# Performance work log

Hardware: AMD Instinct MI355X
Metric: run time of the kernel (lower is better)

The kernel has to match this reference:

```python
import math
import jax, jax.numpy as jnp
import numpy as np

V, D, H, VD, QD, T, HIS, CDD, B = 50000, 300, 16, 16, 200, 20, 50, 5, 256
REPR = H * VD
SCALE = 1.0 / math.sqrt(D)  # original always scales by sqrt(embedding_dim)


def _mhsa_pool(x, Wq, Wv, Wk, bk, qvec):
    """Multi-head self-attention + additive (query-vector) attention pooling.
    x: [B, N, S, F]; Wq: [H, F, F]; Wv: [H, F, VD]; Wk: [REPR, QD]; bk: [QD]; qvec: [QD].
    Returns pooled representation [B, N, REPR].
    Faithful to the per-head loop: heads batched via a leading H axis; concat order
    of per-head value outputs == flatten of (H, VD).
    """
    b, n, s, f = x.shape
    q = jnp.einsum('bnsf,hfe->bhnse', x, Wq)                 # per-head query projection
    attn = jax.nn.softmax(jnp.einsum('bhnse,bnte->bhnst', q, x) * SCALE, axis=-1)
    o = jnp.einsum('bhnst,bntf->bhnsf', attn, x)
    val = jnp.einsum('bhnsf,hfv->bnshv', o, Wv).reshape(b, n, s, H * VD)  # [B,N,S,REPR]
    key = jnp.tanh(val @ Wk + bk)                            # [B,N,S,QD]
    w = jax.nn.softmax(jnp.einsum('q,bnsq->bns', qvec, key) * SCALE, axis=-1)
    return jnp.einsum('bns,bnsr->bnr', w, val)               # [B,N,REPR]


def setup_inputs() -> dict:
    key = jax.random.key(0)
    ks = jax.random.split(key, 13)
    f32 = jnp.float32
    return {
        'candidate_title': jax.random.randint(ks[0], (B, CDD, T), 0, V),
        'clicked_title': jax.random.randint(ks[1], (B, HIS, T), 0, V),
        'embedding': jax.random.normal(ks[2], (V, D), f32) * 0.1,
        'Wq_w': jax.random.normal(ks[3], (H, D, D), f32) * (1.0 / math.sqrt(D)),
        'Wv_w': jax.random.normal(ks[4], (H, D, VD), f32) * (1.0 / math.sqrt(D)),
        'Wk_w': jax.random.normal(ks[5], (REPR, QD), f32) * (1.0 / math.sqrt(REPR)),
        'bk_w': jnp.zeros((QD,), f32),
        'query_words': jax.random.normal(ks[6], (QD,), f32),
        'Wq_n': jax.random.normal(ks[7], (H, REPR, REPR), f32) * (1.0 / math.sqrt(REPR)),
        'Wv_n': jax.random.normal(ks[8], (H, REPR, VD), f32) * (1.0 / math.sqrt(REPR)),
        'Wk_n': jax.random.normal(ks[9], (REPR, QD), f32) * (1.0 / math.sqrt(REPR)),
        'bk_n': jnp.zeros((QD,), f32),
        'query_news': jax.random.normal(ks[10], (QD,), f32),
    }


def reference(candidate_title, clicked_title, embedding, Wq_w, Wv_w, Wk_w, bk_w,
              query_words, Wq_n, Wv_n, Wk_n, bk_n, query_news):
    # news encoder (dropout is identity in eval)
    cdd_emb = embedding[candidate_title]                     # [B,CDD,T,D]
    cdd_reprs = _mhsa_pool(cdd_emb, Wq_w, Wv_w, Wk_w, bk_w, query_words)  # [B,CDD,REPR]
    his_emb = embedding[clicked_title]                       # [B,HIS,T,D]
    his_reprs = _mhsa_pool(his_emb, Wq_w, Wv_w, Wk_w, bk_w, query_words)  # [B,HIS,REPR]
    # user encoder: news-level MHSA + additive pooling over history
    user_repr = _mhsa_pool(his_reprs[:, None], Wq_n, Wv_n, Wk_n, bk_n, query_news)[:, 0]  # [B,REPR]
    # click predictor: dot product, log-softmax over candidates (cdd_size > 1)
    score = jnp.einsum('bcr,br->bc', cdd_reprs, user_repr)   # [B,CDD]
    return jax.nn.log_softmax(score, axis=1)
```

## Files before the change

### kernel.cpp

```cpp
#include <hip/hip_runtime.h>
#include <hip/hip_bf16.h>
#include <math.h>

#define NB 256
#define CDD 5
#define HIS 50
#define NITEMS 55
#define TT 20
#define DD 300
#define NH 16
#define VDIM 16
#define RP 256
#define QDIM 200
#define SCALEF 0.057735026918962584f

typedef __attribute__((ext_vector_type(8)))  short bf16x8;
typedef __attribute__((ext_vector_type(4)))  short short4v;
typedef __attribute__((ext_vector_type(4)))  float f32x4;
typedef __attribute__((ext_vector_type(16))) float f32x16;

#define MFMA16(a,b,c) __builtin_amdgcn_mfma_f32_16x16x32_bf16((a),(b),(c),0,0,0)
#define MFMA32(a,b,c) __builtin_amdgcn_mfma_f32_32x32x16_bf16((a),(b),(c),0,0,0)

__device__ __forceinline__ ushort f2bf(float f) {
    union { float f; unsigned u; } c; c.f = f;
    unsigned u = c.u;
    return (ushort)((u + 0x7fffu + ((u >> 16) & 1u)) >> 16);
}
__device__ __forceinline__ float bf2f(ushort h) {
    union { unsigned u; float f; } c; c.u = ((unsigned)h) << 16;
    return c.f;
}

#define XS  328
#define QS  136
#define VS  264
#define XVS 264
#define XV7 136

__global__ __launch_bounds__(256)
void prep_wqa(const float* __restrict__ Wq, ushort* __restrict__ WqA)
{
    const int TOT = 16 * 102400;
    for (int idx = blockIdx.x * 256 + threadIdx.x; idx < TOT; idx += gridDim.x * 256) {
        const int h  = idx / 102400;
        int r  = idx - h * 102400;
        const int et = r / 10240;  r -= et * 10240;
        const int ks = r / 512;    r -= ks * 512;
        const int ei = r >> 4, ki = r & 15;
        const int e = et * 32 + ei, f = ks * 16 + ki;
        const float v = (e < 300 && f < 300) ? Wq[(h * 300 + f) * 300 + e] : 0.f;
        WqA[idx] = f2bf(v);
    }
}

__global__ __launch_bounds__(256)
void transpose_pad(const float* __restrict__ src, ushort* __restrict__ dst,
                   int R, int C, int src_ld, int Rp, int Cv,
                   long src_ss, long dst_ss)
{
    __shared__ float T[32][33];
    const int r0 = blockIdx.x * 32;
    const int c0 = blockIdx.y * 32;
    const float* s = src + blockIdx.z * src_ss;
    ushort* d = dst + blockIdx.z * dst_ss;
    const int i = threadIdx.x >> 3;
    const int j4 = (threadIdx.x & 7) * 4;
#pragma unroll
    for (int t = 0; t < 4; ++t) {
        const int r = r0 + i, c = c0 + j4 + t;
        T[i][j4 + t] = (r < R && c < C) ? s[(long)r * src_ld + c] : 0.f;
    }
    __syncthreads();
#pragma unroll
    for (int t = 0; t < 4; ++t) {
        const int orow = c0 + i;
        const int ocol = r0 + j4 + t;
        if (orow < Cv && ocol < Rp)
            d[(long)orow * Rp + ocol] = f2bf(T[j4 + t][i]);
    }
}

__global__ __launch_bounds__(256)
void prep_ev(const float* __restrict__ E, const ushort* __restrict__ WvT,
             ushort* __restrict__ EV)
{
    __shared__ ushort Ebf[64 * XS];
    const int tid = threadIdx.x;
    const int r0 = blockIdx.x * 64;
    for (int i = tid; i < (64 * XS) / 2; i += 256) ((unsigned*)Ebf)[i] = 0u;
    __syncthreads();
    for (int idx = tid; idx < 64 * 75; idx += 256) {
        const int row = idx / 75, q = idx - row * 75;
        const int vr = r0 + row;
        if (vr < 50000) {
            const float4 v = ((const float4*)E)[(long)vr * 75 + q];
            short4v p;
            p.x = (short)f2bf(v.x); p.y = (short)f2bf(v.y);
            p.z = (short)f2bf(v.z); p.w = (short)f2bf(v.w);
            *(short4v*)(Ebf + row * XS + q * 4) = p;
        }
    }
    __syncthreads();
    const int w = tid >> 6, l15 = tid & 15, lhi = (tid >> 4) & 3;
    const f32x4 z4 = {0.f, 0.f, 0.f, 0.f};
    for (int n = 0; n < 16; ++n) {
        f32x4 acc = z4;
#pragma unroll
        for (int ks = 0; ks < 10; ++ks) {
            const int off = ks * 32 + lhi * 8;
            const bf16x8 A = *(const bf16x8*)(Ebf + (16 * w + l15) * XS + off);
            const bf16x8 B = *(const bf16x8*)(WvT + (16 * n + l15) * 320 + off);
            acc = MFMA16(A, B, acc);
        }
#pragma unroll
        for (int r = 0; r < 4; ++r) {
            const int row = r0 + 16 * w + lhi * 4 + r;
            if (row < 50000) EV[(long)row * 256 + 16 * n + l15] = f2bf(acc[r]);
        }
    }
}

__device__ __forceinline__ f32x16 zero16() {
    f32x16 z;
#pragma unroll
    for (int i = 0; i < 16; ++i) z[i] = 0.f;
    return z;
}

__device__ __forceinline__ void qc_et3(const ushort* __restrict__ WqAh,
                                       const ushort* Xl, ushort* Qcl,
                                       int et, int jcol, int l31, int hi)
{
    f32x16 acc0 = zero16(), acc1 = zero16(), acc2 = zero16();
    const ushort* abase = WqAh + (et * 20) * 512 + l31 * 16 + hi * 8;
    bf16x8 Abuf[5];
#pragma unroll
    for (int i = 0; i < 5; ++i) Abuf[i] = *(const bf16x8*)(abase + i * 512);
    __builtin_amdgcn_s_setprio(1);
#pragma unroll
    for (int ks = 0; ks < 20; ++ks) {
        const bf16x8 A = Abuf[ks % 5];
        const int xoff = ks * 16 + hi * 8;
        const bf16x8 B0 = *(const bf16x8*)(Xl + (0 * 32 + l31) * XS + xoff);
        acc0 = MFMA32(A, B0, acc0);
        const bf16x8 B1 = *(const bf16x8*)(Xl + (1 * 32 + l31) * XS + xoff);
        acc1 = MFMA32(A, B1, acc1);
        const bf16x8 B2 = *(const bf16x8*)(Xl + (2 * 32 + l31) * XS + xoff);
        acc2 = MFMA32(A, B2, acc2);
        if (ks + 5 < 20) Abuf[ks % 5] = *(const bf16x8*)(abase + (ks + 5) * 512);
    }
    __builtin_amdgcn_s_setprio(0);
#pragma unroll
    for (int m = 0; m < 3; ++m) {
        f32x16 a;
        switch (m) { case 0: a = acc0; break; case 1: a = acc1; break; default: a = acc2; break; }
        if (m == 2 && l31 >= 16) continue;
        ushort* qrow = Qcl + (32 * m + l31) * QS + jcol * 32;
#pragma unroll
        for (int g = 0; g < 4; ++g) {
            short4v p;
            p.x = (short)f2bf(a[4 * g + 0]);
            p.y = (short)f2bf(a[4 * g + 1]);
            p.z = (short)f2bf(a[4 * g + 2]);
            p.w = (short)f2bf(a[4 * g + 3]);
            *(short4v*)(qrow + 8 * g + 4 * hi) = p;
        }
    }
}

template<int NT>
__device__ __forceinline__ void s_chunk(const ushort* Xl, const ushort* Qcl,
                                        f32x16& sacc, int ebase, int i20,
                                        int l31, int hi)
{
    const ushort* xr = Xl + (i20 + l31) * XS + ebase + hi * 8;
    const ushort* qr = Qcl + (i20 + l31) * QS + hi * 8;
#pragma unroll
    for (int kst = 0; kst < 2 * NT; ++kst) {
        const bf16x8 A = *(const bf16x8*)(xr + kst * 16);
        const bf16x8 B = *(const bf16x8*)(qr + kst * 16);
        sacc = MFMA32(A, B, sacc);
    }
}

#define POOLE 39296

__global__ __launch_bounds__(256, 2)
void word_encoder_v7(const int* __restrict__ cddT, const int* __restrict__ hisT,
                     const float* __restrict__ E,
                     const ushort* __restrict__ WqA, const ushort* __restrict__ EV,
                     const ushort* __restrict__ WkT,
                     const float* __restrict__ bk, const float* __restrict__ qv,
                     float* __restrict__ cddR, float* __restrict__ hisR)
{
    __shared__ ushort pool[POOLE];
    __shared__ float  wrf[80];
    __shared__ int    toks[80];
    ushort* Xbf = pool;
    ushort* Qc  = pool + 26240;
    ushort* XVT = pool + 37120;

    const int tid = threadIdx.x;
    const int w   = tid >> 6;
    const int l31 = tid & 31;
    const int hi  = (tid >> 5) & 1;
    const int l15 = tid & 15;
    const int lhi = (tid >> 4) & 3;
    const f32x4 z4 = {0.f, 0.f, 0.f, 0.f};
    const int item = w;
    const int i20  = item * 20;

    for (int i = tid; i < 26240 / 2; i += 256) ((unsigned*)Xbf)[i] = 0u;
    for (int i = tid; i < 2176 / 2; i += 256) ((unsigned*)XVT)[i] = 0u;
    if (tid < 80) {
        wrf[tid] = 0.f;
        const int it_l = tid / 20, t = tid - it_l * 20;
        const int gi = blockIdx.x * 4 + it_l;
        const int b = gi / NITEMS, it = gi - b * NITEMS;
        toks[tid] = (it < CDD) ? cddT[(b * CDD + it) * TT + t]
                               : hisT[(b * HIS + (it - CDD)) * TT + t];
    }
    __syncthreads();

    for (int idx = tid; idx < 80 * 38; idx += 256) {
        const int r = idx / 38, g = idx - r * 38;
        const long base = (long)toks[r] * 300 + g * 8;
        short4v p0, p1;
        if (g < 37) {
            const float4 v0 = *(const float4*)(E + base);
            const float4 v1 = *(const float4*)(E + base + 4);
            p0.x = (short)f2bf(v0.x); p0.y = (short)f2bf(v0.y);
            p0.z = (short)f2bf(v0.z); p0.w = (short)f2bf(v0.w);
            p1.x = (short)f2bf(v1.x); p1.y = (short)f2bf(v1.y);
            p1.z = (short)f2bf(v1.z); p1.w = (short)f2bf(v1.w);
        } else {
            const float4 v0 = *(const float4*)(E + base);
            p0.x = (short)f2bf(v0.x); p0.y = (short)f2bf(v0.y);
            p0.z = (short)f2bf(v0.z); p0.w = (short)f2bf(v0.w);
            p1.x = 0; p1.y = 0; p1.z = 0; p1.w = 0;
        }
        *(short4v*)(Xbf + r * XS + g * 8) = p0;
        *(short4v*)(Xbf + r * XS + g * 8 + 4) = p1;
    }
    __syncthreads();

    unsigned va0=0,va1=0,va2=0,va3=0,va4=0,va5=0,va6=0,va7=0;
    unsigned va8=0,va9=0,va10=0,va11=0,va12=0,va13=0,va14=0,va15=0;
    unsigned vb0=0,vb1=0,vb2=0,vb3=0,vb4=0,vb5=0,vb6=0,vb7=0;
    unsigned vb8=0,vb9=0,vb10=0,vb11=0,vb12=0,vb13=0,vb14=0,vb15=0;
    unsigned vc0=0,vc1=0,vc2=0,vc3=0,vc4=0,vc5=0,vc6=0,vc7=0;
    unsigned vc8=0,vc9=0,vc10=0,vc11=0,vc12=0,vc13=0,vc14=0,vc15=0;
    unsigned vd0=0,vd1=0,vd2=0,vd3=0,vd4=0,vd5=0,vd6=0,vd7=0;
    unsigned vd8=0,vd9=0,vd10=0,vd11=0,vd12=0,vd13=0,vd14=0,vd15=0;

#pragma unroll 1
    for (int h = 0; h < 16; ++h) {
        const ushort* WqAh = WqA + h * 102400;
        f32x16 sacc = zero16();

        if (tid < 160) {
            const int tok = tid >> 1, half = tid & 1;
            const int it2 = tok / 20, lt = tok - it2 * 20;
            const ushort4* src = (const ushort4*)(EV + (long)toks[tok] * 256 + h * 16 + half * 8);
            const ushort4 a = src[0], b2 = src[1];
            ushort* dst0 = XVT + (half * 8) * XV7 + it2 * 32 + lt;
            dst0[0 * XV7] = a.x;  dst0[1 * XV7] = a.y;
            dst0[2 * XV7] = a.z;  dst0[3 * XV7] = a.w;
            dst0[4 * XV7] = b2.x; dst0[5 * XV7] = b2.y;
            dst0[6 * XV7] = b2.z; dst0[7 * XV7] = b2.w;
        }
        qc_et3(WqAh, Xbf, Qc, w, w, l31, hi);
        __syncthreads();
        s_chunk<4>(Xbf, Qc, sacc, 0, i20, l31, hi);
        __syncthreads();

        qc_et3(WqAh, Xbf, Qc, 4 + w, w, l31, hi);
        __syncthreads();
        s_chunk<4>(Xbf, Qc, sacc, 128, i20, l31, hi);
        __syncthreads();

        if (w < 2) qc_et3(WqAh, Xbf, Qc, 8 + w, w, l31, hi);
        __syncthreads();
        s_chunk<2>(Xbf, Qc, sacc, 256, i20, l31, hi);
        __syncthreads();

        float pv[16];
        float vmax = -1e30f;
#pragma unroll
        for (int r = 0; r < 16; ++r) {
            const int t = (r & 3) + 8 * (r >> 2) + 4 * hi;
            const float v = (t < 20) ? sacc[r] * SCALEF : -1e30f;
            pv[r] = v;
            vmax = fmaxf(vmax, v);
        }
        vmax = fmaxf(vmax, __shfl_xor(vmax, 32, 64));
        float psum = 0.f;
#pragma unroll
        for (int r = 0; r < 16; ++r) {
            const int t = (r & 3) + 8 * (r >> 2) + 4 * hi;
            const float e = (t < 20) ? __expf(pv[r] - vmax) : 0.f;
            pv[r] = e;
            psum += e;
        }
        psum += __shfl_xor(psum, 32, 64);
        const float inv = 1.f / psum;
        ushort* Pl = Qc;
        if (l31 < 20) {
            ushort* prow = Pl + (i20 + l31) * QS;
#pragma unroll
            for (int r = 0; r < 16; ++r) {
                const int t = (r & 3) + 8 * (r >> 2) + 4 * hi;
                if (t < 20) prow[t] = f2bf(pv[r] * inv);
            }
        }
        asm volatile("s_waitcnt lgkmcnt(0)" ::: "memory");
        __builtin_amdgcn_sched_barrier(0);

        unsigned plo0, phi0, plo1, phi1;
        {
            const bf16x8 A0 = *(const bf16x8*)(Pl + (i20 + l15) * QS + lhi * 8);
            const bf16x8 B0 = *(const bf16x8*)(XVT + l15 * XV7 + item * 32 + lhi * 8);
            const f32x4 d0 = MFMA16(A0, B0, z4);
            const bf16x8 A1 = *(const bf16x8*)(Pl + (i20 + 16 + l15) * QS + lhi * 8);
            const f32x4 d1 = MFMA16(A1, B0, z4);
            plo0 = ((unsigned)f2bf(d0[1]) << 16) | (unsigned)f2bf(d0[0]);
            phi0 = ((unsigned)f2bf(d0[3]) << 16) | (unsigned)f2bf(d0[2]);
            plo1 = ((unsigned)f2bf(d1[1]) << 16) | (unsigned)f2bf(d1[0]);
            phi1 = ((unsigned)f2bf(d1[3]) << 16) | (unsigned)f2bf(d1[2]);
        }
#define PV_CASE(H) case H: va##H = plo0; vb##H = phi0; vc##H = plo1; vd##H = phi1; break;
        switch (h) {
            PV_CASE(0) PV_CASE(1) PV_CASE(2) PV_CASE(3)
            PV_CASE(4) PV_CASE(5) PV_CASE(6) PV_CASE(7)
            PV_CASE(8) PV_CASE(9) PV_CASE(10) PV_CASE(11)
            PV_CASE(12) PV_CASE(13) PV_CASE(14) PV_CASE(15)
        }
#undef PV_CASE
        __syncthreads();
    }

    ushort* Vlbf = Xbf;
    __syncthreads();
#pragma unroll 1
    for (int h2 = 0; h2 < 16; ++h2) {
        unsigned a = 0, b2 = 0, c = 0, d = 0;
#define UNP_CASE(H) case H: a = va##H; b2 = vb##H; c = vc##H; d = vd##H; break;
        switch (h2) {
            UNP_CASE(0) UNP_CASE(1) UNP_CASE(2) UNP_CASE(3)
            UNP_CASE(4) UNP_CASE(5) UNP_CASE(6) UNP_CASE(7)
            UNP_CASE(8) UNP_CASE(9) UNP_CASE(10) UNP_CASE(11)
            UNP_CASE(12) UNP_CASE(13) UNP_CASE(14) UNP_CASE(15)
        }
#undef UNP_CASE
        ushort* base0 = Vlbf + (i20 + lhi * 4) * VS + h2 * 16 + l15;
        base0[0 * VS] = (ushort)(a & 0xffffu);
        base0[1 * VS] = (ushort)(a >> 16);
        base0[2 * VS] = (ushort)(b2 & 0xffffu);
        base0[3 * VS] = (ushort)(b2 >> 16);
        if (lhi == 0) {
            ushort* base1 = Vlbf + (i20 + 16) * VS + h2 * 16 + l15;
            base1[0 * VS] = (ushort)(c & 0xffffu);
            base1[1 * VS] = (ushort)(c >> 16);
            base1[2 * VS] = (ushort)(d & 0xffffu);
            base1[3 * VS] = (ushort)(d >> 16);
        }
    }
    __syncthreads();

    for (int tile = w; tile < 65; tile += 4) {
        const int m = tile / 13, n = tile - m * 13;
        const int q = 16 * n + l15;
        const float bkq = (q < QDIM) ? bk[q] : 0.f;
        const float qvq = (q < QDIM) ? qv[q] : 0.f;
        f32x4 acc = z4;
#pragma unroll
        for (int ks = 0; ks < 8; ++ks) {
            const int off = ks * 32 + lhi * 8;
            const bf16x8 A = *(const bf16x8*)(Vlbf + (16 * m + l15) * VS + off);
            const bf16x8 B = *(const bf16x8*)(WkT + (16 * n + l15) * 256 + off);
            acc = MFMA16(A, B, acc);
        }
#pragma unroll
        for (int r = 0; r < 4; ++r) {
            float c = qvq * tanhf(acc[r] + bkq);
            c += __shfl_xor(c, 1, 64);
            c += __shfl_xor(c, 2, 64);
            c += __shfl_xor(c, 4, 64);
            c += __shfl_xor(c, 8, 64);
            if (l15 == 0) atomicAdd(&wrf[16 * m + lhi * 4 + r], c);
        }
    }
    __syncthreads();

    if (tid < 4) {
        const int i = tid;
        float m = -1e30f;
        for (int s = 0; s < 20; ++s) m = fmaxf(m, wrf[20 * i + s] * SCALEF);
        float sum = 0.f;
        for (int s = 0; s < 20; ++s) {
            const float e = __expf(wrf[20 * i + s] * SCALEF - m);
            wrf[20 * i + s] = e; sum += e;
        }
        const float invs = 1.f / sum;
        for (int s = 0; s < 20; ++s) wrf[20 * i + s] *= invs;
    }
    __syncthreads();

    for (int idx = tid; idx < 4 * 256; idx += 256) {
        const int i = idx >> 8, r = idx & 255;
        float s = 0.f;
#pragma unroll
        for (int t = 0; t < 20; ++t)
            s += wrf[20 * i + t] * bf2f(Vlbf[(20 * i + t) * VS + r]);
        const int gi = blockIdx.x * 4 + i;
        const int b = gi / NITEMS, it = gi - b * NITEMS;
        float* op = (it < CDD) ? (cddR + (b * CDD + it) * RP)
                               : (hisR + (b * HIS + (it - CDD)) * RP);
        op[r] = s;
    }
}

__device__ __forceinline__ void qc_et(const ushort* __restrict__ WqAh,
                                      const ushort* Xl, ushort* Qcl,
                                      int et, int jcol, int l31, int hi)
{
    f32x16 acc0 = zero16(), acc1 = zero16(), acc2 = zero16(),
           acc3 = zero16(), acc4 = zero16();
    const ushort* abase = WqAh + (et * 20) * 512 + l31 * 16 + hi * 8;
    bf16x8 Abuf[5];
#pragma unroll
    for (int i = 0; i < 5; ++i) Abuf[i] = *(const bf16x8*)(abase + i * 512);
    __builtin_amdgcn_s_setprio(1);
#pragma unroll
    for (int ks = 0; ks < 20; ++ks) {
        const bf16x8 A = Abuf[ks % 5];
        const int xoff = ks * 16 + hi * 8;
        const bf16x8 B0 = *(const bf16x8*)(Xl + (0 * 32 + l31) * XS + xoff);
        acc0 = MFMA32(A, B0, acc0);
        const bf16x8 B1 = *(const bf16x8*)(Xl + (1 * 32 + l31) * XS + xoff);
        acc1 = MFMA32(A, B1, acc1);
        const bf16x8 B2 = *(const bf16x8*)(Xl + (2 * 32 + l31) * XS + xoff);
        acc2 = MFMA32(A, B2, acc2);
        const bf16x8 B3 = *(const bf16x8*)(Xl + (3 * 32 + l31) * XS + xoff);
        acc3 = MFMA32(A, B3, acc3);
        const bf16x8 B4 = *(const bf16x8*)(Xl + (4 * 32 + l31) * XS + xoff);
        acc4 = MFMA32(A, B4, acc4);
        if (ks + 5 < 20) Abuf[ks % 5] = *(const bf16x8*)(abase + (ks + 5) * 512);
    }
    __builtin_amdgcn_s_setprio(0);
#pragma unroll
    for (int m = 0; m < 5; ++m) {
        f32x16 a;
        switch (m) {
            case 0: a = acc0; break; case 1: a = acc1; break;
            case 2: a = acc2; break; case 3: a = acc3; break;
            default: a = acc4; break;
        }
        ushort* qrow = Qcl + (32 * m + l31) * QS + jcol * 32;
#pragma unroll
        for (int g = 0; g < 4; ++g) {
            short4v p;
            p.x = (short)f2bf(a[4 * g + 0]);
            p.y = (short)f2bf(a[4 * g + 1]);
            p.z = (short)f2bf(a[4 * g + 2]);
            p.w = (short)f2bf(a[4 * g + 3]);
            *(short4v*)(qrow + 8 * g + 4 * hi) = p;
        }
    }
}

__global__ __launch_bounds__(512, 2)
void word_encoder_mfma(const int* __restrict__ cddT, const int* __restrict__ hisT,
                       const float* __restrict__ E,
                       const ushort* __restrict__ WqA, const ushort* __restrict__ WvT,
                       const ushort* __restrict__ WkT,
                       const float* __restrict__ bk, const float* __restrict__ qv,
                       float* __restrict__ cddR, float* __restrict__ hisR)
{
    __shared__ ushort Xbf[160 * XS];
    __shared__ ushort Qc[160 * QS];
    __shared__ ushort XVT[16 * XVS];
    __shared__ ushort toks[160];
    __shared__ float  wrf[160];

    const int tid = threadIdx.x;
    const int w   = tid >> 6;
    const int l31 = tid & 31;
    const int hi  = (tid >> 5) & 1;
    const int l15 = tid & 15;
    const int lhi = (tid >> 4) & 3;
    const f32x4 z4 = {0.f, 0.f, 0.f, 0.f};

    for (int i = tid; i < (160 * XS) / 2; i += 512) ((unsigned*)Xbf)[i] = 0u;
    for (int i = tid; i < (16 * XVS) / 2; i += 512) ((unsigned*)XVT)[i] = 0u;
    if (tid < 160) {
        wrf[tid] = 0.f;
        const int it_l = tid / 20, t = tid - it_l * 20;
        const int gi = blockIdx.x * 8 + it_l;
        const int b = gi / NITEMS, it = gi - b * NITEMS;
        const int tk = (it < CDD) ? cddT[(b * CDD + it) * TT + t]
                                  : hisT[(b * HIS + (it - CDD)) * TT + t];
        toks[tid] = (ushort)tk;
    }
    __syncthreads();

    for (int idx = tid; idx < 160 * 38; idx += 512) {
        const int r = idx / 38, g = idx - r * 38;
        const long base = (long)toks[r] * 300 + g * 8;
        short4v p0, p1;
        if (g < 37) {
            const float4 v0 = *(const float4*)(E + base);
            const float4 v1 = *(const float4*)(E + base + 4);
            p0.x = (short)f2bf(v0.x); p0.y = (short)f2bf(v0.y);
            p0.z = (short)f2bf(v0.z); p0.w = (short)f2bf(v0.w);
            p1.x = (short)f2bf(v1.x); p1.y = (short)f2bf(v1.y);
            p1.z = (short)f2bf(v1.z); p1.w = (short)f2bf(v1.w);
        } else {
            const float4 v0 = *(const float4*)(E + base);
            p0.x = (short)f2bf(v0.x); p0.y = (short)f2bf(v0.y);
            p0.z = (short)f2bf(v0.z); p0.w = (short)f2bf(v0.w);
            p1.x = 0; p1.y = 0; p1.z = 0; p1.w = 0;
        }
        *(short4v*)(Xbf + r * XS + g * 8) = p0;
        *(short4v*)(Xbf + r * XS + g * 8 + 4) = p1;
    }
    __syncthreads();

    unsigned va0=0,va1=0,va2=0,va3=0,va4=0,va5=0,va6=0,va7=0;
    unsigned va8=0,va9=0,va10=0,va11=0,va12=0,va13=0,va14=0,va15=0;
    unsigned vb0=0,vb1=0,vb2=0,vb3=0,vb4=0,vb5=0,vb6=0,vb7=0;
    unsigned vb8=0,vb9=0,vb10=0,vb11=0,vb12=0,vb13=0,vb14=0,vb15=0;
    unsigned vc0=0,vc1=0,vc2=0,vc3=0,vc4=0,vc5=0,vc6=0,vc7=0;
    unsigned vc8=0,vc9=0,vc10=0,vc11=0,vc12=0,vc13=0,vc14=0,vc15=0;
    unsigned vd0=0,vd1=0,vd2=0,vd3=0,vd4=0,vd5=0,vd6=0,vd7=0;
    unsigned vd8=0,vd9=0,vd10=0,vd11=0,vd12=0,vd13=0,vd14=0,vd15=0;

    const int item = w;
    const int i20  = item * 20;

#pragma unroll 1
    for (int h = 0; h < 16; ++h) {
        const ushort* WqAh = WqA + h * 102400;
        f32x16 sacc = zero16();

        if (w < 4) {
            qc_et(WqAh, Xbf, Qc, w, w, l31, hi);
        } else {
            for (int tt = w - 4; tt < 10; tt += 4) {
                f32x4 acc = z4;
#pragma unroll
                for (int ks = 0; ks < 10; ++ks) {
                    const int off = ks * 32 + lhi * 8;
                    const bf16x8 A = *(const bf16x8*)(WvT + (h * 16 + l15) * 320 + off);
                    const bf16x8 B = *(const bf16x8*)(Xbf + (tt * 16 + l15) * XS + off);
                    acc = MFMA16(A, B, acc);
                }
                const int t = tt * 16 + l15;
                const int it2 = t / 20, lt = t - it2 * 20;
#pragma unroll
                for (int r = 0; r < 4; ++r)
                    XVT[(lhi * 4 + r) * XVS + it2 * 32 + lt] = f2bf(acc[r]);
            }
        }
        __syncthreads();
        s_chunk<4>(Xbf, Qc, sacc, 0, i20, l31, hi);
        __syncthreads();

        if (w < 4) qc_et(WqAh, Xbf, Qc, 4 + w, w, l31, hi);
        __syncthreads();
        s_chunk<4>(Xbf, Qc, sacc, 128, i20, l31, hi);
        __syncthreads();

        if (w == 0 || w == 2) qc_et(WqAh, Xbf, Qc, 8 + (w >> 1), (w >> 1), l31, hi);
        __syncthreads();
        s_chunk<2>(Xbf, Qc, sacc, 256, i20, l31, hi);
        __syncthreads();

        float sv[16];
        float vmax = -1e30f;
#pragma unroll
        for (int r = 0; r < 16; ++r) {
            const int t = (r & 3) + 8 * (r >> 2) + 4 * hi;
            const float v = (t < 20) ? sacc[r] * SCALEF : -1e30f;
            sv[r] = v;
            vmax = fmaxf(vmax, v);
        }
        vmax = fmaxf(vmax, __shfl_xor(vmax, 32, 64));
        float psum = 0.f;
        float pv[16];
#pragma unroll
        for (int r = 0; r < 16; ++r) {
            const int t = (r & 3) + 8 * (r >> 2) + 4 * hi;
            const float e = (t < 20) ? __expf(sv[r] - vmax) : 0.f;
            pv[r] = e;
            psum += e;
        }
        psum += __shfl_xor(psum, 32, 64);
        const float inv = 1.f / psum;
        ushort* Pl = Qc;
        if (l31 < 20) {
            ushort* prow = Pl + (i20 + l31) * QS;
#pragma unroll
            for (int r = 0; r < 16; ++r) {
                const int t = (r & 3) + 8 * (r >> 2) + 4 * hi;
                if (t < 20) prow[t] = f2bf(pv[r] * inv);
            }
        }
        asm volatile("s_waitcnt lgkmcnt(0)" ::: "memory");
        __builtin_amdgcn_sched_barrier(0);

        unsigned plo0, phi0, plo1, phi1;
        {
            const bf16x8 A0 = *(const bf16x8*)(Pl + (i20 + l15) * QS + lhi * 8);
            const bf16x8 B0 = *(const bf16x8*)(XVT + l15 * XVS + item * 32 + lhi * 8);
            const f32x4 d0 = MFMA16(A0, B0, z4);
            const bf16x8 A1 = *(const bf16x8*)(Pl + (i20 + 16 + l15) * QS + lhi * 8);
            const f32x4 d1 = MFMA16(A1, B0, z4);
            plo0 = ((unsigned)f2bf(d0[1]) << 16) | (unsigned)f2bf(d0[0]);
            phi0 = ((unsigned)f2bf(d0[3]) << 16) | (unsigned)f2bf(d0[2]);
            plo1 = ((unsigned)f2bf(d1[1]) << 16) | (unsigned)f2bf(d1[0]);
            phi1 = ((unsigned)f2bf(d1[3]) << 16) | (unsigned)f2bf(d1[2]);
        }
#define PV_CASE(H) case H: va##H = plo0; vb##H = phi0; vc##H = plo1; vd##H = phi1; break;
        switch (h) {
            PV_CASE(0) PV_CASE(1) PV_CASE(2) PV_CASE(3)
            PV_CASE(4) PV_CASE(5) PV_CASE(6) PV_CASE(7)
            PV_CASE(8) PV_CASE(9) PV_CASE(10) PV_CASE(11)
            PV_CASE(12) PV_CASE(13) PV_CASE(14) PV_CASE(15)
        }
#undef PV_CASE
        __syncthreads();
    }

    ushort* Vlbf = Xbf;
    __syncthreads();
#pragma unroll 1
    for (int h2 = 0; h2 < 16; ++h2) {
        unsigned a = 0, b2 = 0, c = 0, d = 0;
#define UNP_CASE(H) case H: a = va##H; b2 = vb##H; c = vc##H; d = vd##H; break;
        switch (h2) {
            UNP_CASE(0) UNP_CASE(1) UNP_CASE(2) UNP_CASE(3)
            UNP_CASE(4) UNP_CASE(5) UNP_CASE(6) UNP_CASE(7)
            UNP_CASE(8) UNP_CASE(9) UNP_CASE(10) UNP_CASE(11)
            UNP_CASE(12) UNP_CASE(13) UNP_CASE(14) UNP_CASE(15)
        }
#undef UNP_CASE
        ushort* base0 = Vlbf + (i20 + lhi * 4) * VS + h2 * 16 + l15;
        base0[0 * VS] = (ushort)(a & 0xffffu);
        base0[1 * VS] = (ushort)(a >> 16);
        base0[2 * VS] = (ushort)(b2 & 0xffffu);
        base0[3 * VS] = (ushort)(b2 >> 16);
        if (lhi == 0) {
            ushort* base1 = Vlbf + (i20 + 16) * VS + h2 * 16 + l15;
            base1[0 * VS] = (ushort)(c & 0xffffu);
            base1[1 * VS] = (ushort)(c >> 16);
            base1[2 * VS] = (ushort)(d & 0xffffu);
            base1[3 * VS] = (ushort)(d >> 16);
        }
    }
    __syncthreads();

    for (int tile = w; tile < 130; tile += 8) {
        const int m = tile / 13, n = tile - m * 13;
        const int q = 16 * n + l15;
        const float bkq = (q < QDIM) ? bk[q] : 0.f;
        const float qvq = (q < QDIM) ? qv[q] : 0.f;
        f32x4 acc = z4;
#pragma unroll
        for (int ks = 0; ks < 8; ++ks) {
            const int off = ks * 32 + lhi * 8;
            const bf16x8 A = *(const bf16x8*)(Vlbf + (16 * m + l15) * VS + off);
            const bf16x8 B = *(const bf16x8*)(WkT + (16 * n + l15) * 256 + off);
            acc = MFMA16(A, B, acc);
        }
#pragma unroll
        for (int r = 0; r < 4; ++r) {
            float c = qvq * tanhf(acc[r] + bkq);
            c += __shfl_xor(c, 1, 64);
            c += __shfl_xor(c, 2, 64);
            c += __shfl_xor(c, 4, 64);
            c += __shfl_xor(c, 8, 64);
            if (l15 == 0) atomicAdd(&wrf[16 * m + lhi * 4 + r], c);
        }
    }
    __syncthreads();

    if (tid < 8) {
        const int i = tid;
        float m = -1e30f;
        for (int s = 0; s < 20; ++s) m = fmaxf(m, wrf[20 * i + s] * SCALEF);
        float sum = 0.f;
        for (int s = 0; s < 20; ++s) {
            const float e = __expf(wrf[20 * i + s] * SCALEF - m);
            wrf[20 * i + s] = e; sum += e;
        }
        const float invs = 1.f / sum;
        for (int s = 0; s < 20; ++s) wrf[20 * i + s] *= invs;
    }
    __syncthreads();

    for (int idx = tid; idx < 8 * 256; idx += 512) {
        const int i = idx >> 8, r = idx & 255;
        float s = 0.f;
#pragma unroll
        for (int t = 0; t < 20; ++t)
            s += wrf[20 * i + t] * bf2f(Vlbf[(20 * i + t) * VS + r]);
        const int gi = blockIdx.x * 8 + i;
        const int b = gi / NITEMS, it = gi - b * NITEMS;
        float* op = (it < CDD) ? (cddR + (b * CDD + it) * RP)
                               : (hisR + (b * HIS + (it - CDD)) * RP);
        op[r] = s;
    }
}

#define US   264
#define UTS  72
#define UXVS 72
#define UVS  264

__global__ __launch_bounds__(512, 2)
void user_encoder_mfma(const float* __restrict__ hisR,
                       const ushort* __restrict__ WqnT, const ushort* __restrict__ WvnT,
                       const ushort* __restrict__ WknT,
                       const float* __restrict__ bk, const float* __restrict__ qv,
                       float* __restrict__ userR)
{
    __shared__ ushort Xu[64 * US];
    __shared__ ushort Qu[64 * US];
    __shared__ ushort XVTu[16 * UXVS];
    __shared__ ushort Atu[64 * UTS];
    __shared__ ushort Vlu[64 * UVS];
    __shared__ float  wru[64];

    const int tid = threadIdx.x;
    const int w   = tid >> 6;
    const int l15 = tid & 15;
    const int lhi = (tid >> 4) & 3;
    const f32x4 z4 = {0.f, 0.f, 0.f, 0.f};

    for (int i = tid; i < (64 * US) / 2; i += 512) ((unsigned*)Xu)[i] = 0u;
    for (int i = tid; i < (64 * UTS) / 2; i += 512) ((unsigned*)Atu)[i] = 0u;
    for (int i = tid; i < (64 * UVS) / 2; i += 512) ((unsigned*)Vlu)[i] = 0u;
    if (tid < 64) wru[tid] = 0.f;
    __syncthreads();

    const float* xp = hisR + (long)blockIdx.x * (HIS * RP);
    for (int idx = tid; idx < 50 * 64; idx += 512) {
        const int s = idx >> 6, q = idx & 63;
        const float4 v = ((const float4*)xp)[idx];
        short4v p;
        p.x = (short)f2bf(v.x); p.y = (short)f2bf(v.y);
        p.z = (short)f2bf(v.z); p.w = (short)f2bf(v.w);
        *(short4v*)(Xu + s * US + q * 4) = p;
    }
    __syncthreads();

#pragma unroll 1
    for (int h = 0; h < 16; ++h) {
        const ushort* Wqh = WqnT + h * 65536;
        for (int t8 = w; t8 < 64; t8 += 8) {
            const int et = t8 >> 2, st = t8 & 3;
            f32x4 acc = z4;
#pragma unroll
            for (int ks = 0; ks < 8; ++ks) {
                const int off = ks * 32 + lhi * 8;
                const bf16x8 A = *(const bf16x8*)(Wqh + (16 * et + l15) * 256 + off);
                const bf16x8 B = *(const bf16x8*)(Xu + (16 * st + l15) * US + off);
                acc = MFMA16(A, B, acc);
            }
            short4v p;
            p.x = (short)f2bf(acc[0]); p.y = (short)f2bf(acc[1]);
            p.z = (short)f2bf(acc[2]); p.w = (short)f2bf(acc[3]);
            *(short4v*)(Qu + (16 * st + l15) * US + 16 * et + lhi * 4) = p;
        }
        __syncthreads();

        if (w < 4) {
            f32x4 a[4] = {z4, z4, z4, z4};
#pragma unroll
            for (int ks = 0; ks < 8; ++ks) {
                const int off = ks * 32 + lhi * 8;
                const bf16x8 qa = *(const bf16x8*)(Qu + (16 * w + l15) * US + off);
#pragma unroll
                for (int n = 0; n < 4; ++n)
                    a[n] = MFMA16(qa, *(const bf16x8*)(Xu + (16 * n + l15) * US + off), a[n]);
            }
#pragma unroll
            for (int r = 0; r < 4; ++r) {
                const int srow = 16 * w + lhi * 4 + r;
                float v[4];
                float m = -1e30f;
#pragma unroll
                for (int n = 0; n < 4; ++n) {
                    const int t = 16 * n + l15;
                    v[n] = (t < HIS) ? a[n][r] * SCALEF : -1e30f;
                    m = fmaxf(m, v[n]);
                }
                m = fmaxf(m, __shfl_xor(m, 1, 64));
                m = fmaxf(m, __shfl_xor(m, 2, 64));
                m = fmaxf(m, __shfl_xor(m, 4, 64));
                m = fmaxf(m, __shfl_xor(m, 8, 64));
                float p[4]; float sum = 0.f;
#pragma unroll
                for (int n = 0; n < 4; ++n) {
                    const int t = 16 * n + l15;
                    p[n] = (t < HIS) ? __expf(v[n] - m) : 0.f;
                    sum += p[n];
                }
                sum += __shfl_xor(sum, 1, 64);
                sum += __shfl_xor(sum, 2, 64);
                sum += __shfl_xor(sum, 4, 64);
                sum += __shfl_xor(sum, 8, 64);
                const float inv = 1.f / sum;
                if (srow < HIS) {
#pragma unroll
                    for (int n = 0; n < 4; ++n)
                        Atu[srow * UTS + 16 * n + l15] = f2bf(p[n] * inv);
                }
            }
        } else {
            const int j = w - 4;
            f32x4 acc = z4;
#pragma unroll
            for (int ks = 0; ks < 8; ++ks) {
                const int off = ks * 32 + lhi * 8;
                const bf16x8 A = *(const bf16x8*)(Xu + (16 * j + l15) * US + off);
                const bf16x8 B = *(const bf16x8*)(WvnT + (h * 16 + l15) * 256 + off);
                acc = MFMA16(A, B, acc);
            }
#pragma unroll
            for (int r = 0; r < 4; ++r)
                XVTu[l15 * UXVS + 16 * j + lhi * 4 + r] = f2bf(acc[r]);
        }
        __syncthreads();

        if (w < 4) {
            f32x4 acc = z4;
#pragma unroll
            for (int ks = 0; ks < 2; ++ks) {
                const int off = ks * 32 + lhi * 8;
                const bf16x8 A = *(const bf16x8*)(Atu + (16 * w + l15) * UTS + off);
                const bf16x8 B = *(const bf16x8*)(XVTu + l15 * UXVS + off);
                acc = MFMA16(A, B, acc);
            }
#pragma unroll
            for (int r = 0; r < 4; ++r) {
                const int srow = 16 * w + lhi * 4 + r;
                if (srow < HIS) Vlu[srow * UVS + h * 16 + l15] = f2bf(acc[r]);
            }
        }
        __syncthreads();
    }

    for (int tile = w; tile < 52; tile += 8) {
        const int m = tile / 13, n = tile - m * 13;
        const int q = 16 * n + l15;
        const float bkq = (q < QDIM) ? bk[q] : 0.f;
        const float qvq = (q < QDIM) ? qv[q] : 0.f;
        f32x4 acc = z4;
#pragma unroll
        for (int ks = 0; ks < 8; ++ks) {
            const int off = ks * 32 + lhi * 8;
            const bf16x8 A = *(const bf16x8*)(Vlu + (16 * m + l15) * UVS + off);
            const bf16x8 B = *(const bf16x8*)(WknT + (16 * n + l15) * 256 + off);
            acc = MFMA16(A, B, acc);
        }
#pragma unroll
        for (int r = 0; r < 4; ++r) {
            float c = qvq * tanhf(acc[r] + bkq);
            c += __shfl_xor(c, 1, 64);
            c += __shfl_xor(c, 2, 64);
            c += __shfl_xor(c, 4, 64);
            c += __shfl_xor(c, 8, 64);
            const int srow = 16 * m + lhi * 4 + r;
            if (l15 == 0 && srow < HIS) atomicAdd(&wru[srow], c);
        }
    }
    __syncthreads();
    if (tid == 0) {
        float m = -1e30f;
        for (int s = 0; s < HIS; ++s) m = fmaxf(m, wru[s] * SCALEF);
        float sum = 0.f;
        for (int s = 0; s < HIS; ++s) {
            const float e = __expf(wru[s] * SCALEF - m);
            wru[s] = e; sum += e;
        }
        const float inv = 1.f / sum;
        for (int s = 0; s < HIS; ++s) wru[s] *= inv;
    }
    __syncthreads();
    if (tid < 256) {
        float s = 0.f;
        for (int t = 0; t < HIS; ++t) s += wru[t] * bf2f(Vlu[t * UVS + tid]);
        userR[blockIdx.x * RP + tid] = s;
    }
}

#define FP2 257
#define CHW 129
__global__ __launch_bounds__(512)
void user_encoder_fp32(const float* __restrict__ hisR,
                       const float* __restrict__ Wq, const float* __restrict__ Wv,
                       const float* __restrict__ Wk, const float* __restrict__ bk,
                       const float* __restrict__ qv,
                       float* __restrict__ userR)
{
    __shared__ float Xs[HIS + 1][FP2];
    __shared__ float Vl[HIS][FP2];
    __shared__ float Qcf[HIS + 1][CHW];
    __shared__ float Sm[HIS][HIS + 2];
    __shared__ float XVh[HIS][VDIM + 1];
    __shared__ float wr[HIS];

    const int tid = threadIdx.x;
    const int b = blockIdx.x;
    const float* xp = hisR + b * (HIS * RP);
    for (int i = tid; i < HIS * RP; i += 512) {
        const int s = i >> 8, f = i & 255;
        Xs[s][f] = xp[i];
    }
    __syncthreads();
    for (int h = 0; h < NH; ++h) {
        for (int chunk = 0; chunk < 2; ++chunk) {
            __syncthreads();
            const int e0 = chunk * 128;
            {
                const int sg = tid >> 7, et = tid & 127;
                const int s0 = sg * 13 - (sg == 3 ? 1 : 0);
                const float* wq = Wq + h * (RP * RP) + e0 + et;
                float acc[13] = {};
                for (int f = 0; f < RP; ++f) {
                    const float w = wq[f * RP];
#pragma unroll
                    for (int i = 0; i < 13; ++i) acc[i] += Xs[s0 + i][f] * w;
                }
#pragma unroll
                for (int i = 0; i < 13; ++i) Qcf[s0 + i][et] = acc[i];
            }
            __syncthreads();
            for (int o = tid; o < HIS * HIS; o += 512) {
                const int s = o / HIS, t = o - s * HIS;
                float acc = (chunk == 0) ? 0.f : Sm[s][t];
                for (int e = 0; e < 128; ++e) acc += Qcf[s][e] * Xs[t][e0 + e];
                Sm[s][t] = acc;
            }
        }
        __syncthreads();
        if (tid < HIS) {
            const int s = tid;
            float m = -1e30f;
            for (int t = 0; t < HIS; ++t) m = fmaxf(m, Sm[s][t]);
            m *= SCALEF;
            float sum = 0.f;
            for (int t = 0; t < HIS; ++t) { const float e = __expf(Sm[s][t] * SCALEF - m); Sm[s][t] = e; sum += e; }
            const float inv = 1.f / sum;
            for (int t = 0; t < HIS; ++t) Sm[s][t] *= inv;
        }
        for (int o = tid; o < HIS * VDIM; o += 512) {
            const int t = o >> 4, v = o & 15;
            const float* wp = Wv + h * (RP * VDIM) + v;
            float acc = 0.f;
            for (int f = 0; f < RP; ++f) acc += Xs[t][f] * wp[f * VDIM];
            XVh[t][v] = acc;
        }
        __syncthreads();
        for (int o = tid; o < HIS * VDIM; o += 512) {
            const int s = o >> 4, v = o & 15;
            float acc = 0.f;
            for (int t = 0; t < HIS; ++t) acc += Sm[s][t] * XVh[t][v];
            Vl[s][h * VDIM + v] = acc;
        }
    }
    __syncthreads();
    {
        const int s = tid >> 3, g = tid & 7;
        float part = 0.f;
        if (s < HIS) {
            for (int q = g; q < QDIM; q += 8) {
                float acc = bk[q];
                const float* wp = Wk + q;
                for (int r = 0; r < RP; ++r) acc += Vl[s][r] * wp[r * QDIM];
                part += qv[q] * tanhf(acc);
            }
        }
        part += __shfl_down(part, 1, 64);
        part += __shfl_down(part, 2, 64);
        part += __shfl_down(part, 4, 64);
        if (g == 0 && s < HIS) wr[s] = part * SCALEF;
    }
    __syncthreads();
    if (tid == 0) {
        float m = -1e30f;
        for (int s = 0; s < HIS; ++s) m = fmaxf(m, wr[s]);
        float sum = 0.f;
        for (int s = 0; s < HIS; ++s) { const float e = __expf(wr[s] - m); wr[s] = e; sum += e; }
        const float inv = 1.f / sum;
        for (int s = 0; s < HIS; ++s) wr[s] *= inv;
    }
    __syncthreads();
    float* up = userR + b * RP;
    for (int r = tid; r < RP; r += 512) {
        float acc = 0.f;
        for (int s = 0; s < HIS; ++s) acc += wr[s] * Vl[s][r];
        up[r] = acc;
    }
}

__global__ __launch_bounds__(64)
void score_kernel(const float* __restrict__ cddR, const float* __restrict__ userR,
                  float* __restrict__ out)
{
    const int b = blockIdx.x;
    const int lane = threadIdx.x;
    const float* u = userR + b * RP;
    float sc[CDD];
#pragma unroll
    for (int c = 0; c < CDD; ++c) {
        const float* cr = cddR + (b * CDD + c) * RP;
        float part = 0.f;
        for (int r = lane; r < RP; r += 64) part += cr[r] * u[r];
#pragma unroll
        for (int off = 32; off > 0; off >>= 1) part += __shfl_down(part, off, 64);
        sc[c] = part;
    }
    if (lane == 0) {
        float m = -1e30f;
#pragma unroll
        for (int c = 0; c < CDD; ++c) m = fmaxf(m, sc[c]);
        float sum = 0.f;
#pragma unroll
        for (int c = 0; c < CDD; ++c) sum += __expf(sc[c] - m);
        const float lse = m + logf(sum);
#pragma unroll
        for (int c = 0; c < CDD; ++c) out[b * CDD + c] = sc[c] - lse;
    }
}

extern "C" void kernel_launch(void* const* d_in, const int* in_sizes, int n_in,
                              void* d_out, int out_size, void* d_ws, size_t ws_size,
                              hipStream_t stream) {
    const int*   cddT = (const int*)d_in[0];
    const int*   hisT = (const int*)d_in[1];
    const float* E    = (const float*)d_in[2];
    const float* Wq_w = (const float*)d_in[3];
    const float* Wv_w = (const float*)d_in[4];
    const float* Wk_w = (const float*)d_in[5];
    const float* bk_w = (const float*)d_in[6];
    const float* q_w  = (const float*)d_in[7];
    const float* Wq_n = (const float*)d_in[8];
    const float* Wv_n = (const float*)d_in[9];
    const float* Wk_n = (const float*)d_in[10];
    const float* bk_n = (const float*)d_in[11];
    const float* q_n  = (const float*)d_in[12];
    float* out = (float*)d_out;

    char* wsb = (char*)d_ws;
    float*  cdd_reprs = (float*)(wsb + 0);
    float*  his_reprs = (float*)(wsb + 1310720);
    float*  user_repr = (float*)(wsb + 14417920);
    ushort* WqA  = (ushort*)(wsb + 14680064);
    ushort* WvT  = (ushort*)(wsb + 17956864);
    ushort* WkT  = (ushort*)(wsb + 18120704);
    ushort* WqnT = (ushort*)(wsb + 18227200);
    ushort* WvnT = (ushort*)(wsb + 20324352);
    ushort* WknT = (ushort*)(wsb + 20455424);
    ushort* EV   = (ushort*)(wsb + 20561920);
    const bool mid  = ws_size >= 20561920ULL + 2335232ULL;
    const bool big  = ws_size >= 46161920ULL;

    prep_wqa<<<dim3(2048), 256, 0, stream>>>(Wq_w, WqA);
    transpose_pad<<<dim3(10, 1, 16), 256, 0, stream>>>(Wv_w, WvT, 300, 16, 16, 320, 16, 4800, 5120);
    transpose_pad<<<dim3(8, 7, 1), 256, 0, stream>>>(Wk_w, WkT, 256, 200, 200, 256, 208, 0, 0);
    if (mid) {
        transpose_pad<<<dim3(8, 8, 16), 256, 0, stream>>>(Wq_n, WqnT, 256, 256, 256, 256, 256, 65536, 65536);
        transpose_pad<<<dim3(8, 1, 16), 256, 0, stream>>>(Wv_n, WvnT, 256, 16, 16, 256, 16, 4096, 4096);
        transpose_pad<<<dim3(8, 7, 1), 256, 0, stream>>>(Wk_n, WknT, 256, 200, 200, 256, 208, 0, 0);
    }

    if (big) {
        prep_ev<<<dim3(782), 256, 0, stream>>>(E, WvT, EV);
        word_encoder_v7<<<dim3(NB * NITEMS / 4), dim3(256), 0, stream>>>(
            cddT, hisT, E, WqA, EV, WkT, bk_w, q_w, cdd_reprs, his_reprs);
    } else {
        word_encoder_mfma<<<dim3(NB * NITEMS / 8), dim3(512), 0, stream>>>(
            cddT, hisT, E, WqA, WvT, WkT, bk_w, q_w, cdd_reprs, his_reprs);
    }
    if (mid)
        user_encoder_mfma<<<dim3(NB), dim3(512), 0, stream>>>(
            his_reprs, WqnT, WvnT, WknT, bk_n, q_n, user_repr);
    else
        user_encoder_fp32<<<dim3(NB), dim3(512), 0, stream>>>(
            his_reprs, Wq_n, Wv_n, Wk_n, bk_n, q_n, user_repr);
    score_kernel<<<dim3(NB), dim3(64), 0, stream>>>(cdd_reprs, user_repr, out);
}
```

Measured before the change: 2.131 ms.

## Shrink word-encoder blocks to two items with 128 threads

Replaces the four-item, 256-thread word encoder with a two-item, 128-thread variant. Shared memory drops to about half, so more blocks can be resident per CU, and the Q projection now uses two MFMA tiles per wave, with the second tile padded from 8 rows. Row indices are remapped so padded lanes read duplicate rows, which removes wasted MFMA rows. The risk is that each block reloads the per-head Wq weights for fewer items, which lowers weight reuse and doubles the block count.

```diff
diff --git a/kernel.cpp b/kernel.cpp
--- a/kernel.cpp
+++ b/kernel.cpp
@@ -36,7 +36,7 @@
 #define QS  136
 #define VS  264
 #define XVS 264
-#define XV7 136
+#define XV8 72
 
 __global__ __launch_bounds__(256)
 void prep_wqa(const float* __restrict__ Wq, ushort* __restrict__ WqA)
@@ -128,34 +128,33 @@
     return z;
 }
 
-__device__ __forceinline__ void qc_et3(const ushort* __restrict__ WqAh,
+__device__ __forceinline__ void qc_et2(const ushort* __restrict__ WqAh,
                                        const ushort* Xl, ushort* Qcl,
                                        int et, int jcol, int l31, int hi)
 {
-    f32x16 acc0 = zero16(), acc1 = zero16(), acc2 = zero16();
+    f32x16 acc0 = zero16(), acc1 = zero16();
     const ushort* abase = WqAh + (et * 20) * 512 + l31 * 16 + hi * 8;
     bf16x8 Abuf[5];
 #pragma unroll
     for (int i = 0; i < 5; ++i) Abuf[i] = *(const bf16x8*)(abase + i * 512);
+    const int brow0 = l31;
+    const int brow1 = 32 + (l31 & 7);
     __builtin_amdgcn_s_setprio(1);
 #pragma unroll
     for (int ks = 0; ks < 20; ++ks) {
         const bf16x8 A = Abuf[ks % 5];
         const int xoff = ks * 16 + hi * 8;
-        const bf16x8 B0 = *(const bf16x8*)(Xl + (0 * 32 + l31) * XS + xoff);
+        const bf16x8 B0 = *(const bf16x8*)(Xl + brow0 * XS + xoff);
         acc0 = MFMA32(A, B0, acc0);
-        const bf16x8 B1 = *(const bf16x8*)(Xl + (1 * 32 + l31) * XS + xoff);
+        const bf16x8 B1 = *(const bf16x8*)(Xl + brow1 * XS + xoff);
         acc1 = MFMA32(A, B1, acc1);
-        const bf16x8 B2 = *(const bf16x8*)(Xl + (2 * 32 + l31) * XS + xoff);
-        acc2 = MFMA32(A, B2, acc2);
         if (ks + 5 < 20) Abuf[ks % 5] = *(const bf16x8*)(abase + (ks + 5) * 512);
     }
     __builtin_amdgcn_s_setprio(0);
 #pragma unroll
-    for (int m = 0; m < 3; ++m) {
-        f32x16 a;
-        switch (m) { case 0: a = acc0; break; case 1: a = acc1; break; default: a = acc2; break; }
-        if (m == 2 && l31 >= 16) continue;
+    for (int m = 0; m < 2; ++m) {
+        f32x16 a = (m == 0) ? acc0 : acc1;
+        if (m == 1 && l31 >= 8) continue;
         ushort* qrow = Qcl + (32 * m + l31) * QS + jcol * 32;
 #pragma unroll
         for (int g = 0; g < 4; ++g) {
@@ -170,12 +169,13 @@
 }
 
 template<int NT>
-__device__ __forceinline__ void s_chunk(const ushort* Xl, const ushort* Qcl,
-                                        f32x16& sacc, int ebase, int i20,
-                                        int l31, int hi)
+__device__ __forceinline__ void s_chunk8(const ushort* Xl, const ushort* Qcl,
+                                         f32x16& sacc, int ebase, int i20,
+                                         int l31, int hi)
 {
-    const ushort* xr = Xl + (i20 + l31) * XS + ebase + hi * 8;
-    const ushort* qr = Qcl + (i20 + l31) * QS + hi * 8;
+    const int rr = i20 + ((l31 < 20) ? l31 : (l31 - 20));
+    const ushort* xr = Xl + rr * XS + ebase + hi * 8;
+    const ushort* qr = Qcl + rr * QS + hi * 8;
 #pragma unroll
     for (int kst = 0; kst < 2 * NT; ++kst) {
         const bf16x8 A = *(const bf16x8*)(xr + kst * 16);
@@ -184,22 +184,22 @@
     }
 }
 
-#define POOLE 39296
-
-__global__ __launch_bounds__(256, 2)
-void word_encoder_v7(const int* __restrict__ cddT, const int* __restrict__ hisT,
+#define POOLE8 19712
+
+__global__ __launch_bounds__(128, 2)
+void word_encoder_v8(const int* __restrict__ cddT, const int* __restrict__ hisT,
                      const float* __restrict__ E,
                      const ushort* __restrict__ WqA, const ushort* __restrict__ EV,
                      const ushort* __restrict__ WkT,
                      const float* __restrict__ bk, const float* __restrict__ qv,
                      float* __restrict__ cddR, float* __restrict__ hisR)
 {
-    __shared__ ushort pool[POOLE];
-    __shared__ float  wrf[80];
-    __shared__ int    toks[80];
+    __shared__ ushort pool[POOLE8];
+    __shared__ float  wrf[40];
+    __shared__ int    toks[40];
     ushort* Xbf = pool;
-    ushort* Qc  = pool + 26240;
-    ushort* XVT = pool + 37120;
+    ushort* Qc  = pool + 13120;
+    ushort* XVT = pool + 18560;
 
     const int tid = threadIdx.x;
     const int w   = tid >> 6;
@@ -211,19 +211,19 @@
     const int item = w;
     const int i20  = item * 20;
 
-    for (int i = tid; i < 26240 / 2; i += 256) ((unsigned*)Xbf)[i] = 0u;
-    for (int i = tid; i < 2176 / 2; i += 256) ((unsigned*)XVT)[i] = 0u;
-    if (tid < 80) {
+    for (int i = tid; i < 13120 / 2; i += 128) ((unsigned*)Xbf)[i] = 0u;
+    for (int i = tid; i < 1152 / 2; i += 128) ((unsigned*)XVT)[i] = 0u;
+    if (tid < 40) {
         wrf[tid] = 0.f;
         const int it_l = tid / 20, t = tid - it_l * 20;
-        const int gi = blockIdx.x * 4 + it_l;
+        const int gi = blockIdx.x * 2 + it_l;
         const int b = gi / NITEMS, it = gi - b * NITEMS;
         toks[tid] = (it < CDD) ? cddT[(b * CDD + it) * TT + t]
                                : hisT[(b * HIS + (it - CDD)) * TT + t];
     }
     __syncthreads();
 
-    for (int idx = tid; idx < 80 * 38; idx += 256) {
+    for (int idx = tid; idx < 40 * 38; idx += 128) {
         const int r = idx / 38, g = idx - r * 38;
         const long base = (long)toks[r] * 300 + g * 8;
         short4v p0, p1;
@@ -259,30 +259,32 @@
         const ushort* WqAh = WqA + h * 102400;
         f32x16 sacc = zero16();
 
-        if (tid < 160) {
+        if (tid < 80) {
             const int tok = tid >> 1, half = tid & 1;
             const int it2 = tok / 20, lt = tok - it2 * 20;
             const ushort4* src = (const ushort4*)(EV + (long)toks[tok] * 256 + h * 16 + half * 8);
             const ushort4 a = src[0], b2 = src[1];
-            ushort* dst0 = XVT + (half * 8) * XV7 + it2 * 32 + lt;
-            dst0[0 * XV7] = a.x;  dst0[1 * XV7] = a.y;
-            dst0[2 * XV7] = a.z;  dst0[3 * XV7] = a.w;
-            dst0[4 * XV7] = b2.x; dst0[5 * XV7] = b2.y;
-            dst0[6 * XV7] = b2.z; dst0[7 * XV7] = b2.w;
-        }
-        qc_et3(WqAh, Xbf, Qc, w, w, l31, hi);
-        __syncthreads();
-        s_chunk<4>(Xbf, Qc, sacc, 0, i20, l31, hi);
-        __syncthreads();
-
-        qc_et3(WqAh, Xbf, Qc, 4 + w, w, l31, hi);
-        __syncthreads();
-        s_chunk<4>(Xbf, Qc, sacc, 128, i20, l31, hi);
-        __syncthreads();
-
-        if (w < 2) qc_et3(WqAh, Xbf, Qc, 8 + w, w, l31, hi);
-        __syncthreads();
-        s_chunk<2>(Xbf, Qc, sacc, 256, i20, l31, hi);
+            ushort* dst0 = XVT + (half * 8) * XV8 + it2 * 32 + lt;
+            dst0[0 * XV8] = a.x;  dst0[1 * XV8] = a.y;
+            dst0[2 * XV8] = a.z;  dst0[3 * XV8] = a.w;
+            dst0[4 * XV8] = b2.x; dst0[5 * XV8] = b2.y;
+            dst0[6 * XV8] = b2.z; dst0[7 * XV8] = b2.w;
+        }
+        qc_et2(WqAh, Xbf, Qc, 2 * w,     2 * w,     l31, hi);
+        qc_et2(WqAh, Xbf, Qc, 2 * w + 1, 2 * w + 1, l31, hi);
+        __syncthreads();
+        s_chunk8<4>(Xbf, Qc, sacc, 0, i20, l31, hi);
+        __syncthreads();
+
+        qc_et2(WqAh, Xbf, Qc, 4 + 2 * w,     2 * w,     l31, hi);
+        qc_et2(WqAh, Xbf, Qc, 4 + 2 * w + 1, 2 * w + 1, l31, hi);
+        __syncthreads();
+        s_chunk8<4>(Xbf, Qc, sacc, 128, i20, l31, hi);
+        __syncthreads();
+
+        qc_et2(WqAh, Xbf, Qc, 8 + w, w, l31, hi);
+        __syncthreads();
+        s_chunk8<2>(Xbf, Qc, sacc, 256, i20, l31, hi);
         __syncthreads();
 
         float pv[16];
@@ -319,10 +321,11 @@
 
         unsigned plo0, phi0, plo1, phi1;
         {
+            const int r1 = i20 + 16 + ((l15 < 4) ? l15 : 0);
             const bf16x8 A0 = *(const bf16x8*)(Pl + (i20 + l15) * QS + lhi * 8);
-            const bf16x8 B0 = *(const bf16x8*)(XVT + l15 * XV7 + item * 32 + lhi * 8);
+            const bf16x8 B0 = *(const bf16x8*)(XVT + l15 * XV8 + item * 32 + lhi * 8);
             const f32x4 d0 = MFMA16(A0, B0, z4);
-            const bf16x8 A1 = *(const bf16x8*)(Pl + (i20 + 16 + l15) * QS + lhi * 8);
+            const bf16x8 A1 = *(const bf16x8*)(Pl + r1 * QS + lhi * 8);
             const f32x4 d1 = MFMA16(A1, B0, z4);
             plo0 = ((unsigned)f2bf(d0[1]) << 16) | (unsigned)f2bf(d0[0]);
             phi0 = ((unsigned)f2bf(d0[3]) << 16) | (unsigned)f2bf(d0[2]);
@@ -368,16 +371,18 @@
     }
     __syncthreads();
 
-    for (int tile = w; tile < 65; tile += 4) {
+    for (int tile = w; tile < 39; tile += 2) {
         const int m = tile / 13, n = tile - m * 13;
         const int q = 16 * n + l15;
         const float bkq = (q < QDIM) ? bk[q] : 0.f;
         const float qvq = (q < QDIM) ? qv[q] : 0.f;
+        int arow = 16 * m + l15;
+        if (arow >= 40) arow -= 8;
         f32x4 acc = z4;
 #pragma unroll
         for (int ks = 0; ks < 8; ++ks) {
             const int off = ks * 32 + lhi * 8;
-            const bf16x8 A = *(const bf16x8*)(Vlbf + (16 * m + l15) * VS + off);
+            const bf16x8 A = *(const bf16x8*)(Vlbf + arow * VS + off);
             const bf16x8 B = *(const bf16x8*)(WkT + (16 * n + l15) * 256 + off);
             acc = MFMA16(A, B, acc);
         }
@@ -388,12 +393,13 @@
             c += __shfl_xor(c, 2, 64);
             c += __shfl_xor(c, 4, 64);
             c += __shfl_xor(c, 8, 64);
-            if (l15 == 0) atomicAdd(&wrf[16 * m + lhi * 4 + r], c);
-        }
-    }
-    __syncthreads();
-
-    if (tid < 4) {
+            const int srow = 16 * m + lhi * 4 + r;
+            if (l15 == 0 && srow < 40) atomicAdd(&wrf[srow], c);
+        }
+    }
+    __syncthreads();
+
+    if (tid < 2) {
         const int i = tid;
         float m = -1e30f;
         for (int s = 0; s < 20; ++s) m = fmaxf(m, wrf[20 * i + s] * SCALEF);
@@ -407,13 +413,13 @@
     }
     __syncthreads();
 
-    for (int idx = tid; idx < 4 * 256; idx += 256) {
+    for (int idx = tid; idx < 2 * 256; idx += 128) {
         const int i = idx >> 8, r = idx & 255;
         float s = 0.f;
 #pragma unroll
         for (int t = 0; t < 20; ++t)
             s += wrf[20 * i + t] * bf2f(Vlbf[(20 * i + t) * VS + r]);
-        const int gi = blockIdx.x * 4 + i;
+        const int gi = blockIdx.x * 2 + i;
         const int b = gi / NITEMS, it = gi - b * NITEMS;
         float* op = (it < CDD) ? (cddR + (b * CDD + it) * RP)
                                : (hisR + (b * HIS + (it - CDD)) * RP);
@@ -467,6 +473,21 @@
             p.w = (short)f2bf(a[4 * g + 3]);
             *(short4v*)(qrow + 8 * g + 4 * hi) = p;
         }
+    }
+}
+
+template<int NT>
+__device__ __forceinline__ void s_chunk(const ushort* Xl, const ushort* Qcl,
+                                        f32x16& sacc, int ebase, int i20,
+                                        int l31, int hi)
+{
+    const ushort* xr = Xl + (i20 + l31) * XS + ebase + hi * 8;
+    const ushort* qr = Qcl + (i20 + l31) * QS + hi * 8;
+#pragma unroll
+    for (int kst = 0; kst < 2 * NT; ++kst) {
+        const bf16x8 A = *(const bf16x8*)(xr + kst * 16);
+        const bf16x8 B = *(const bf16x8*)(qr + kst * 16);
+        sacc = MFMA32(A, B, sacc);
     }
 }
 
@@ -1080,7 +1101,7 @@
 
     if (big) {
         prep_ev<<<dim3(782), 256, 0, stream>>>(E, WvT, EV);
-        word_encoder_v7<<<dim3(NB * NITEMS / 4), dim3(256), 0, stream>>>(
+        word_encoder_v8<<<dim3(NB * NITEMS / 2), dim3(128), 0, stream>>>(
             cddT, hisT, E, WqA, EV, WkT, bk_w, q_w, cdd_reprs, his_reprs);
     } else {
         word_encoder_mfma<<<dim3(NB * NITEMS / 8), dim3(512), 0, stream>>>(
```

Result: slower. 2.639 ms (+23.8%).
